# Optimization experiments

Hardware: AMD Instinct MI355X
Metric: run time of the kernel (lower is better)

The kernel has to match this reference:

```python
import jax, jax.numpy as jnp
import numpy as np

N_NODES = 50000
NEG_SLOPE = 0.2
EPS = 1e-16


def _gat_conv(x, src, dst, W, a_src, a_dst, bias, heads, out_c, concat):
    """PyG-style GATConv (self-loops assumed already added to src/dst)."""
    N = x.shape[0]
    h = (x @ W).reshape(N, heads, out_c)                 # [N,H,C]
    s_src = jnp.sum(h * a_src, axis=-1)                  # [N,H]
    s_dst = jnp.sum(h * a_dst, axis=-1)                  # [N,H]
    e = jax.nn.leaky_relu(s_src[src] + s_dst[dst], NEG_SLOPE)  # [E,H]
    # segment softmax over incoming edges of each dst node
    m = jax.ops.segment_max(e, dst, num_segments=N)      # [N,H]
    e = jnp.exp(e - m[dst])
    z = jax.ops.segment_sum(e, dst, num_segments=N)      # [N,H]
    alpha = e / (z[dst] + EPS)                           # [E,H]
    out = jax.ops.segment_sum(h[src] * alpha[:, :, None], dst, num_segments=N)  # [N,H,C]
    if concat:
        out = out.reshape(N, heads * out_c)
    else:
        out = out.mean(axis=1)
    return out + bias


def setup_inputs() -> dict:
    key = jax.random.key(0)
    ks = jax.random.split(key, 12)
    N, E, nfeat, nhid, nclass = N_NODES, 800000, 512, 256, 40
    heads, head_dim = 4, nhid // 4
    g = lambda k, shape, fan: (jax.random.normal(k, shape, jnp.float32) * (1.0 / np.sqrt(fan)))
    return {
        "x": jax.random.normal(ks[0], (N, nfeat), jnp.float32),
        "adj": jax.random.randint(ks[1], (2, E), 0, N, jnp.int64),
        "W1": g(ks[2], (nfeat, heads * head_dim), nfeat),
        "att_src1": g(ks[3], (heads, head_dim), head_dim),
        "att_dst1": g(ks[4], (heads, head_dim), head_dim),
        "b1": jnp.zeros((heads * head_dim,), jnp.float32),
        "W2": g(ks[5], (nhid, nclass), nhid),
        "att_src2": g(ks[6], (1, nclass), nclass),
        "att_dst2": g(ks[7], (1, nclass), nclass),
        "b2": jnp.zeros((nclass,), jnp.float32),
    }


def reference(x, adj, W1, att_src1, att_dst1, b1, W2, att_src2, att_dst2, b2):
    N = x.shape[0]
    loops = jnp.arange(N, dtype=adj.dtype)
    src = jnp.concatenate([adj[0], loops])   # PyG GATConv add_self_loops=True
    dst = jnp.concatenate([adj[1], loops])
    h = _gat_conv(x, src, dst, W1, att_src1, att_dst1, b1, heads=4, out_c=64, concat=True)
    h = jax.nn.relu(h)
    # dropout: eval mode => identity
    out = _gat_conv(h, src, dst, W2, att_src2, att_dst2, b2, heads=1, out_c=40, concat=False)
    return out
```

## Files before the change

kernel.cpp:

```cpp
#include <hip/hip_runtime.h>
#include <hip/hip_bf16.h>
#include <math.h>

#define NFEAT 512
#define NHID 256
#define HEADS 4
#define HDIM 64
#define NCLASS 40
#define NEG_SLOPE 0.2f
#define EPS_Z 1e-16f

typedef short bf16x8 __attribute__((ext_vector_type(8)));
typedef float f32x4 __attribute__((ext_vector_type(4)));

__device__ __forceinline__ float lrelu(float x) {
  return x > 0.f ? x : NEG_SLOPE * x;
}

__device__ __forceinline__ ushort f2bf(float f) {
  union { float f; uint u; } c; c.f = f;
  uint u = c.u;
  uint r = u + 0x7FFFu + ((u >> 16) & 1u);
  return (ushort)(r >> 16);
}
__device__ __forceinline__ float bf2f(ushort h) {
  union { uint u; float f; } c; c.u = ((uint)h) << 16;
  return c.f;
}

__device__ __forceinline__ uint cvtpk(float lo, float hi) {
  uint r;
  asm("v_cvt_pk_bf16_f32 %0, %1, %2" : "=v"(r) : "v"(lo), "v"(hi));
  return r;
}


__global__ void count_kernel(const int* __restrict__ dstv, int E, int* __restrict__ counts) {
  int i = blockIdx.x * blockDim.x + threadIdx.x;
  if (i < E) atomicAdd(&counts[dstv[i]], 1);
}

__global__ __launch_bounds__(1024) void scan_a(const int* __restrict__ counts,
    int* __restrict__ excl, int* __restrict__ bsum, int n) {
  __shared__ int tmp[1024];
  int t = threadIdx.x;
  int i = blockIdx.x * 1024 + t;
  int v = (i < n) ? counts[i] : 0;
  tmp[t] = v;
  __syncthreads();
  for (int off = 1; off < 1024; off <<= 1) {
    int u = (t >= off) ? tmp[t - off] : 0;
    __syncthreads();
    tmp[t] += u;
    __syncthreads();
  }
  if (i < n) excl[i] = tmp[t] - v;
  if (t == 1023) bsum[blockIdx.x] = tmp[t];
}

__global__ __launch_bounds__(1024) void scan_b(int* __restrict__ bsum, int nb) {
  __shared__ int tmp[1024];
  int t = threadIdx.x;
  tmp[t] = (t < nb) ? bsum[t] : 0;
  __syncthreads();
  for (int off = 1; off < 1024; off <<= 1) {
    int u = (t >= off) ? tmp[t - off] : 0;
    __syncthreads();
    tmp[t] += u;
    __syncthreads();
  }
  if (t < nb) bsum[t] = tmp[t];
}

__global__ void scan_c(const int* __restrict__ excl, const int* __restrict__ bsum_incl,
    int* __restrict__ row_off, int* __restrict__ cursor, int n, int E) {
  int i = blockIdx.x * blockDim.x + threadIdx.x;
  if (i < n) {
    int b = i >> 10;
    int off = (b > 0) ? bsum_incl[b - 1] : 0;
    int v = excl[i] + off;
    row_off[i] = v;
    cursor[i] = v;
  }
  if (i == 0) row_off[n] = E;
}

__global__ void scatter_kernel(const int* __restrict__ srcv, const int* __restrict__ dstv,
                               int E, int* __restrict__ cursor, int* __restrict__ edge_src) {
  int i = blockIdx.x * blockDim.x + threadIdx.x;
  if (i < E) {
    int pos = atomicAdd(&cursor[dstv[i]], 1);
    edge_src[pos] = srcv[i];
  }
}


__global__ __launch_bounds__(64) void wprep_kernel(const float* __restrict__ W,
    ushort* __restrict__ Bh) {
  int fb = blockIdx.x;
  int ct = fb >> 4, ks = fb & 15;
  int l = threadIdx.x;
  int g = l >> 4, rr = l & 15;
  uint hw[4];
  #pragma unroll
  for (int p = 0; p < 4; ++p) {
    ushort h2v[2];
    #pragma unroll
    for (int q = 0; q < 2; ++q) {
      int e = p * 2 + q;
      int k = ks * 32 + 4 * g + (e & 3) + 16 * (e >> 2);
      int col = ct * 16 + rr;
      h2v[q] = f2bf(W[k * NHID + col]);
    }
    hw[p] = (uint)h2v[0] | ((uint)h2v[1] << 16);
  }
  size_t o = ((size_t)fb * 64 + l) * 8;
  uint4 hv; hv.x = hw[0]; hv.y = hw[1]; hv.z = hw[2]; hv.w = hw[3];
  *(uint4*)&Bh[o] = hv;
}


__global__ __launch_bounds__(256, 4) void gemm1_mfma(const float* __restrict__ A,
    const ushort* __restrict__ Bh,
    const float* __restrict__ asrc, const float* __restrict__ adst,
    ushort* __restrict__ h1b, float* __restrict__ ssrc1, float* __restrict__ sdst1,
    int M) {
  __shared__ float A_s[2][64 * 64];
  const int tid = threadIdx.x;
  const int lane = tid & 63;
  const int wc = tid >> 6;
  const int g = lane >> 4, rr = lane & 15;
  const int row0 = blockIdx.x * 64;

  f32x4 acc[4][4] = {};

  auto stage = [&](int ki, int buf) {
    #pragma unroll
    for (int j = 0; j < 4; ++j) {
      int grp = wc * 4 + j;
      int s = grp * 64 + lane;
      int r = s >> 4;
      int us = s & 15;
      int ud = us ^ (r & 7);
      int gr = row0 + r;
      if (gr >= M) gr = M - 1;
      const float* src = &A[(size_t)gr * NFEAT + ki * 64 + ud * 4];
      float* dst = &A_s[buf][grp * 256];
      __builtin_amdgcn_global_load_lds(
          (const __attribute__((address_space(1))) float*)src,
          (__attribute__((address_space(3))) float*)dst, 16, 0, 0);
    }
  };

  stage(0, 0);
  __syncthreads();

  for (int ki = 0; ki < 8; ++ki) {
    const int cur = ki & 1;
    if (ki < 7) stage(ki + 1, cur ^ 1);

    #pragma unroll
    for (int kk = 0; kk < 2; ++kk) {
      const int ks = ki * 2 + kk;
      bf16x8 bhf[4];
      #pragma unroll
      for (int ni = 0; ni < 4; ++ni) {
        int ct = wc * 4 + ni;
        size_t bidx = ((size_t)(ct * 16 + ks) * 64 + lane) * 8;
        bhf[ni] = *(const bf16x8*)&Bh[bidx];
      }
      #pragma unroll
      for (int mi = 0; mi < 4; ++mi) {
        int row = mi * 16 + rr;
        int u0 = (8 * kk + g) ^ (row & 7);
        int u1 = (8 * kk + 4 + g) ^ (row & 7);
        f32x4 lo = *(const f32x4*)&A_s[cur][row * 64 + u0 * 4];
        f32x4 hi = *(const f32x4*)&A_s[cur][row * 64 + u1 * 4];
        uint w0 = cvtpk(lo[0], lo[1]);
        uint w1 = cvtpk(lo[2], lo[3]);
        uint w2 = cvtpk(hi[0], hi[1]);
        uint w3 = cvtpk(hi[2], hi[3]);
        union { uint u[4]; bf16x8 v; } af;
        af.u[0] = w0; af.u[1] = w1; af.u[2] = w2; af.u[3] = w3;
        #pragma unroll
        for (int ni = 0; ni < 4; ++ni) {
          acc[mi][ni] = __builtin_amdgcn_mfma_f32_16x16x32_bf16(af.v, bhf[ni], acc[mi][ni], 0, 0, 0);
        }
      }
    }
    __syncthreads();
  }

  float a_s[4], a_d[4];
  #pragma unroll
  for (int ni = 0; ni < 4; ++ni) {
    a_s[ni] = asrc[wc * 64 + ni * 16 + rr];
    a_d[ni] = adst[wc * 64 + ni * 16 + rr];
  }

  #pragma unroll
  for (int mi = 0; mi < 4; ++mi) {
    #pragma unroll
    for (int j = 0; j < 4; ++j) {
      int r = row0 + mi * 16 + g * 4 + j;
      bool ok = r < M;
      float ps = 0.f, pd = 0.f;
      #pragma unroll
      for (int ni = 0; ni < 4; ++ni) {
        float v = acc[mi][ni][j];
        ps += v * a_s[ni];
        pd += v * a_d[ni];
        if (ok) h1b[(size_t)r * NHID + wc * 64 + ni * 16 + rr] = f2bf(v);
      }
      #pragma unroll
      for (int m = 1; m < 16; m <<= 1) {
        ps += __shfl_xor(ps, m, 64);
        pd += __shfl_xor(pd, m, 64);
      }
      if (ok && rr == 0) {
        ssrc1[r * HEADS + wc] = ps;
        sdst1[r * HEADS + wc] = pd;
      }
    }
  }
}


__global__ __launch_bounds__(256) void gemm2_fused(const ushort* __restrict__ A,
    const float* __restrict__ B, const float* __restrict__ asrc,
    const float* __restrict__ adst, ushort* __restrict__ h2b,
    float* __restrict__ ssrc2, float* __restrict__ sdst2, int M) {
  __shared__ float As[16][64 + 1];
  __shared__ float Bs[16][68];
  const int tid = threadIdx.x;
  const int tx = tid & 15, ty = tid >> 4;
  const int row0 = blockIdx.x * 64;
  float acc[4][4] = {};

  const int la_r = tid >> 2;
  const int la_k = (tid & 3) * 4;
  const int lb_r = tid >> 4;
  const int lb_c = (tid & 15) * 4;

  for (int k0 = 0; k0 < NHID; k0 += 16) {
    float a0 = 0.f, a1 = 0.f, a2 = 0.f, a3 = 0.f;
    int ar = row0 + la_r;
    if (ar < M) {
      ushort4 uv = *(const ushort4*)&A[(size_t)ar * NHID + k0 + la_k];
      a0 = bf2f(uv.x); a1 = bf2f(uv.y); a2 = bf2f(uv.z); a3 = bf2f(uv.w);
    }
    As[la_k + 0][la_r] = a0;
    As[la_k + 1][la_r] = a1;
    As[la_k + 2][la_r] = a2;
    As[la_k + 3][la_r] = a3;

    float4 bv = make_float4(0.f, 0.f, 0.f, 0.f);
    const float* Brow = &B[(size_t)(k0 + lb_r) * NCLASS];
    if (lb_c + 3 < NCLASS) bv = *(const float4*)&Brow[lb_c];
    *(float4*)&Bs[lb_r][lb_c] = bv;
    __syncthreads();

    #pragma unroll
    for (int k = 0; k < 16; ++k) {
      float x0 = As[k][ty * 4 + 0];
      float x1 = As[k][ty * 4 + 1];
      float x2 = As[k][ty * 4 + 2];
      float x3 = As[k][ty * 4 + 3];
      float4 b = *(const float4*)&Bs[k][tx * 4];
      acc[0][0] += x0 * b.x; acc[0][1] += x0 * b.y; acc[0][2] += x0 * b.z; acc[0][3] += x0 * b.w;
      acc[1][0] += x1 * b.x; acc[1][1] += x1 * b.y; acc[1][2] += x1 * b.z; acc[1][3] += x1 * b.w;
      acc[2][0] += x2 * b.x; acc[2][1] += x2 * b.y; acc[2][2] += x2 * b.z; acc[2][3] += x2 * b.w;
      acc[3][0] += x3 * b.x; acc[3][1] += x3 * b.y; acc[3][2] += x3 * b.z; acc[3][3] += x3 * b.w;
    }
    __syncthreads();
  }

  const int cbase = tx * 4;
  const bool cok = cbase + 3 < NCLASS;
  float4 av_s = make_float4(0.f, 0.f, 0.f, 0.f);
  float4 av_d = make_float4(0.f, 0.f, 0.f, 0.f);
  if (cok) {
    av_s = *(const float4*)&asrc[cbase];
    av_d = *(const float4*)&adst[cbase];
  }

  #pragma unroll
  for (int i = 0; i < 4; ++i) {
    int r = row0 + ty * 4 + i;
    bool ok = r < M;
    float ps = acc[i][0] * av_s.x + acc[i][1] * av_s.y + acc[i][2] * av_s.z + acc[i][3] * av_s.w;
    float pd = acc[i][0] * av_d.x + acc[i][1] * av_d.y + acc[i][2] * av_d.z + acc[i][3] * av_d.w;
    #pragma unroll
    for (int m = 1; m < 16; m <<= 1) {
      ps += __shfl_xor(ps, m, 64);
      pd += __shfl_xor(pd, m, 64);
    }
    if (ok && cok) {
      ushort4 o;
      o.x = f2bf(acc[i][0]); o.y = f2bf(acc[i][1]);
      o.z = f2bf(acc[i][2]); o.w = f2bf(acc[i][3]);
      *(ushort4*)&h2b[(size_t)r * NCLASS + cbase] = o;
    }
    if (ok && tx == 0) { ssrc2[r] = ps; sdst2[r] = pd; }
  }
}


__global__ __launch_bounds__(64) void agg1_kernel(const ushort* __restrict__ h1b,
    const float* __restrict__ s_src, const float* __restrict__ s_dst,
    const int* __restrict__ row_off, const int* __restrict__ edge_src,
    const float* __restrict__ b1, ushort* __restrict__ hrelu_b) {
  int v = blockIdx.x;
  int l = threadIdx.x;
  int head = l >> 4;
  int c = l * 4;
  float sdv = s_dst[v * HEADS + head];

  float w = __expf(lrelu(s_src[v * HEADS + head] + sdv));
  ushort4 hv = *(const ushort4*)&h1b[(size_t)v * NHID + c];
  float4 acc = make_float4(w * bf2f(hv.x), w * bf2f(hv.y), w * bf2f(hv.z), w * bf2f(hv.w));
  float z = w;

  int i = row_off[v], end = row_off[v + 1];
  for (; i + 3 < end; i += 4) {
    int u0 = edge_src[i + 0];
    int u1 = edge_src[i + 1];
    int u2 = edge_src[i + 2];
    int u3 = edge_src[i + 3];
    float e0 = s_src[u0 * HEADS + head];
    float e1 = s_src[u1 * HEADS + head];
    float e2 = s_src[u2 * HEADS + head];
    float e3 = s_src[u3 * HEADS + head];
    ushort4 r0 = *(const ushort4*)&h1b[(size_t)u0 * NHID + c];
    ushort4 r1 = *(const ushort4*)&h1b[(size_t)u1 * NHID + c];
    ushort4 r2 = *(const ushort4*)&h1b[(size_t)u2 * NHID + c];
    ushort4 r3 = *(const ushort4*)&h1b[(size_t)u3 * NHID + c];
    float w0 = __expf(lrelu(e0 + sdv));
    float w1 = __expf(lrelu(e1 + sdv));
    float w2 = __expf(lrelu(e2 + sdv));
    float w3 = __expf(lrelu(e3 + sdv));
    acc.x += w0 * bf2f(r0.x) + w1 * bf2f(r1.x) + w2 * bf2f(r2.x) + w3 * bf2f(r3.x);
    acc.y += w0 * bf2f(r0.y) + w1 * bf2f(r1.y) + w2 * bf2f(r2.y) + w3 * bf2f(r3.y);
    acc.z += w0 * bf2f(r0.z) + w1 * bf2f(r1.z) + w2 * bf2f(r2.z) + w3 * bf2f(r3.z);
    acc.w += w0 * bf2f(r0.w) + w1 * bf2f(r1.w) + w2 * bf2f(r2.w) + w3 * bf2f(r3.w);
    z += (w0 + w1) + (w2 + w3);
  }
  for (; i < end; ++i) {
    int u = edge_src[i];
    float wu = __expf(lrelu(s_src[u * HEADS + head] + sdv));
    ushort4 hu = *(const ushort4*)&h1b[(size_t)u * NHID + c];
    acc.x += wu * bf2f(hu.x);
    acc.y += wu * bf2f(hu.y);
    acc.z += wu * bf2f(hu.z);
    acc.w += wu * bf2f(hu.w);
    z += wu;
  }
  float inv = 1.f / (z + EPS_Z);
  float4 bb = *(const float4*)&b1[c];
  ushort4 o;
  o.x = f2bf(fmaxf(acc.x * inv + bb.x, 0.f));
  o.y = f2bf(fmaxf(acc.y * inv + bb.y, 0.f));
  o.z = f2bf(fmaxf(acc.z * inv + bb.z, 0.f));
  o.w = f2bf(fmaxf(acc.w * inv + bb.w, 0.f));
  *(ushort4*)&hrelu_b[(size_t)v * NHID + c] = o;
}

__global__ __launch_bounds__(64) void agg2_kernel(const ushort* __restrict__ h2b,
    const float* __restrict__ s_src, const float* __restrict__ s_dst,
    const int* __restrict__ row_off, const int* __restrict__ edge_src,
    const float* __restrict__ b2, float* __restrict__ out) {
  int v = blockIdx.x;
  int l = threadIdx.x;
  bool act = l < NCLASS;
  float sdv = s_dst[v];

  float w = __expf(lrelu(s_src[v] + sdv));
  float acc = act ? w * bf2f(h2b[(size_t)v * NCLASS + l]) : 0.f;
  float z = w;

  int i = row_off[v], end = row_off[v + 1];
  for (; i + 3 < end; i += 4) {
    int u0 = edge_src[i + 0];
    int u1 = edge_src[i + 1];
    int u2 = edge_src[i + 2];
    int u3 = edge_src[i + 3];
    float e0 = s_src[u0];
    float e1 = s_src[u1];
    float e2 = s_src[u2];
    float e3 = s_src[u3];
    ushort p0 = 0, p1 = 0, p2 = 0, p3 = 0;
    if (act) {
      p0 = h2b[(size_t)u0 * NCLASS + l];
      p1 = h2b[(size_t)u1 * NCLASS + l];
      p2 = h2b[(size_t)u2 * NCLASS + l];
      p3 = h2b[(size_t)u3 * NCLASS + l];
    }
    float w0 = __expf(lrelu(e0 + sdv));
    float w1 = __expf(lrelu(e1 + sdv));
    float w2 = __expf(lrelu(e2 + sdv));
    float w3 = __expf(lrelu(e3 + sdv));
    if (act) acc += w0 * bf2f(p0) + w1 * bf2f(p1) + w2 * bf2f(p2) + w3 * bf2f(p3);
    z += (w0 + w1) + (w2 + w3);
  }
  for (; i < end; ++i) {
    int u = edge_src[i];
    float wu = __expf(lrelu(s_src[u] + sdv));
    if (act) acc += wu * bf2f(h2b[(size_t)u * NCLASS + l]);
    z += wu;
  }
  if (act) out[(size_t)v * NCLASS + l] = acc / (z + EPS_Z) + b2[l];
}


extern "C" void kernel_launch(void* const* d_in, const int* in_sizes, int n_in,
                              void* d_out, int out_size, void* d_ws, size_t ws_size,
                              hipStream_t stream) {
  const float* x   = (const float*)d_in[0];
  const int*   adj = (const int*)d_in[1];
  const float* W1  = (const float*)d_in[2];
  const float* as1 = (const float*)d_in[3];
  const float* ad1 = (const float*)d_in[4];
  const float* b1  = (const float*)d_in[5];
  const float* W2  = (const float*)d_in[6];
  const float* as2 = (const float*)d_in[7];
  const float* ad2 = (const float*)d_in[8];
  const float* b2  = (const float*)d_in[9];
  float* out = (float*)d_out;

  const int N = in_sizes[0] / NFEAT;
  const int E = in_sizes[1] / 2;

  char* ws = (char*)d_ws;
  size_t off = 0;
  auto alloc = [&](size_t bytes) -> void* {
    void* p = ws + off;
    off = (off + bytes + 255) & ~(size_t)255;
    return p;
  };
  ushort* h1b    = (ushort*)alloc((size_t)N * NHID * 2);
  ushort* hrelub = (ushort*)alloc((size_t)N * NHID * 2);
  ushort* h2b    = (ushort*)alloc((size_t)N * NCLASS * 2);
  float* ssrc1   = (float*)alloc((size_t)N * HEADS * 4);
  float* sdst1   = (float*)alloc((size_t)N * HEADS * 4);
  float* ssrc2   = (float*)alloc((size_t)N * 4);
  float* sdst2   = (float*)alloc((size_t)N * 4);
  int* counts    = (int*)alloc((size_t)N * 4);
  int* cursor    = (int*)alloc((size_t)N * 4);
  int* row_off   = (int*)alloc((size_t)(N + 1) * 4);
  int* edge_src  = (int*)alloc((size_t)E * 4);
  int* excl      = (int*)alloc((size_t)N * 4);
  int* bsum      = (int*)alloc((size_t)1024 * 4);
  ushort* whp    = (ushort*)alloc((size_t)NFEAT * NHID * 2);
  (void)ws_size;

  const int* srcv = adj;
  const int* dstv = adj + E;
  const int nb = (N + 1023) / 1024;

  wprep_kernel<<<256, 64, 0, stream>>>(W1, whp);

  hipMemsetAsync(counts, 0, (size_t)N * 4, stream);
  count_kernel<<<(E + 255) / 256, 256, 0, stream>>>(dstv, E, counts);
  scan_a<<<nb, 1024, 0, stream>>>(counts, excl, bsum, N);
  scan_b<<<1, 1024, 0, stream>>>(bsum, nb);
  scan_c<<<(N + 255) / 256, 256, 0, stream>>>(excl, bsum, row_off, cursor, N, E);
  scatter_kernel<<<(E + 255) / 256, 256, 0, stream>>>(srcv, dstv, E, cursor, edge_src);

  gemm1_mfma<<<(N + 63) / 64, 256, 0, stream>>>(x, whp, as1, ad1, h1b, ssrc1, sdst1, N);
  agg1_kernel<<<N, 64, 0, stream>>>(h1b, ssrc1, sdst1, row_off, edge_src, b1, hrelub);

  gemm2_fused<<<(N + 63) / 64, 256, 0, stream>>>(hrelub, W2, as2, ad2, h2b, ssrc2, sdst2, N);
  agg2_kernel<<<N, 64, 0, stream>>>(h2b, ssrc2, sdst2, row_off, edge_src, b2, out);
}
```

Baseline: 274.8 us.

## Cooperatively load edge indices and attention weights across lanes, broadcast via shuffles

In both aggregation kernels, each lane of the wavefront (or of its 16-lane head group) now loads one edge index and computes one exp attention weight for a chunk of edges. The index and weight are then broadcast with cross-lane shuffles while every lane gathers the feature rows. The softmax denominator becomes a per-lane partial that is reduced with xor-shuffles at the end. This removes the redundant per-lane loads of edge_src and s_src and the repeated exp computations. In exchange it adds shuffle traffic and an extra reduction.

```diff
diff --git a/kernel.cpp b/kernel.cpp
--- a/kernel.cpp
+++ b/kernel.cpp
@@ -313,49 +313,59 @@
   int v = blockIdx.x;
   int l = threadIdx.x;
   int head = l >> 4;
+  int elane = l & 15;
   int c = l * 4;
   float sdv = s_dst[v * HEADS + head];
 
-  float w = __expf(lrelu(s_src[v * HEADS + head] + sdv));
+  float wself = __expf(lrelu(s_src[v * HEADS + head] + sdv));
   ushort4 hv = *(const ushort4*)&h1b[(size_t)v * NHID + c];
-  float4 acc = make_float4(w * bf2f(hv.x), w * bf2f(hv.y), w * bf2f(hv.z), w * bf2f(hv.w));
-  float z = w;
+  float4 acc = make_float4(wself * bf2f(hv.x), wself * bf2f(hv.y),
+                           wself * bf2f(hv.z), wself * bf2f(hv.w));
+  float zp = (elane == 0) ? wself : 0.f;
 
   int i = row_off[v], end = row_off[v + 1];
-  for (; i + 3 < end; i += 4) {
-    int u0 = edge_src[i + 0];
-    int u1 = edge_src[i + 1];
-    int u2 = edge_src[i + 2];
-    int u3 = edge_src[i + 3];
-    float e0 = s_src[u0 * HEADS + head];
-    float e1 = s_src[u1 * HEADS + head];
-    float e2 = s_src[u2 * HEADS + head];
-    float e3 = s_src[u3 * HEADS + head];
-    ushort4 r0 = *(const ushort4*)&h1b[(size_t)u0 * NHID + c];
-    ushort4 r1 = *(const ushort4*)&h1b[(size_t)u1 * NHID + c];
-    ushort4 r2 = *(const ushort4*)&h1b[(size_t)u2 * NHID + c];
-    ushort4 r3 = *(const ushort4*)&h1b[(size_t)u3 * NHID + c];
-    float w0 = __expf(lrelu(e0 + sdv));
-    float w1 = __expf(lrelu(e1 + sdv));
-    float w2 = __expf(lrelu(e2 + sdv));
-    float w3 = __expf(lrelu(e3 + sdv));
-    acc.x += w0 * bf2f(r0.x) + w1 * bf2f(r1.x) + w2 * bf2f(r2.x) + w3 * bf2f(r3.x);
-    acc.y += w0 * bf2f(r0.y) + w1 * bf2f(r1.y) + w2 * bf2f(r2.y) + w3 * bf2f(r3.y);
-    acc.z += w0 * bf2f(r0.z) + w1 * bf2f(r1.z) + w2 * bf2f(r2.z) + w3 * bf2f(r3.z);
-    acc.w += w0 * bf2f(r0.w) + w1 * bf2f(r1.w) + w2 * bf2f(r2.w) + w3 * bf2f(r3.w);
-    z += (w0 + w1) + (w2 + w3);
-  }
-  for (; i < end; ++i) {
-    int u = edge_src[i];
-    float wu = __expf(lrelu(s_src[u * HEADS + head] + sdv));
-    ushort4 hu = *(const ushort4*)&h1b[(size_t)u * NHID + c];
-    acc.x += wu * bf2f(hu.x);
-    acc.y += wu * bf2f(hu.y);
-    acc.z += wu * bf2f(hu.z);
-    acc.w += wu * bf2f(hu.w);
-    z += wu;
-  }
-  float inv = 1.f / (z + EPS_Z);
+  for (; i < end; i += 16) {
+    int cnt = end - i;
+    if (cnt > 16) cnt = 16;
+    bool val = elane < cnt;
+    int u = edge_src[val ? (i + elane) : i];
+    float wl = 0.f;
+    if (val) wl = __expf(lrelu(s_src[u * HEADS + head] + sdv));
+    zp += wl;
+
+    int e = 0;
+    for (; e + 3 < cnt; e += 4) {
+      int u0 = __shfl(u, e + 0);
+      int u1 = __shfl(u, e + 1);
+      int u2 = __shfl(u, e + 2);
+      int u3 = __shfl(u, e + 3);
+      float w0 = __shfl(wl, (l & 48) | (e + 0));
+      float w1 = __shfl(wl, (l & 48) | (e + 1));
+      float w2 = __shfl(wl, (l & 48) | (e + 2));
+      float w3 = __shfl(wl, (l & 48) | (e + 3));
+      ushort4 r0 = *(const ushort4*)&h1b[(size_t)u0 * NHID + c];
+      ushort4 r1 = *(const ushort4*)&h1b[(size_t)u1 * NHID + c];
+      ushort4 r2 = *(const ushort4*)&h1b[(size_t)u2 * NHID + c];
+      ushort4 r3 = *(const ushort4*)&h1b[(size_t)u3 * NHID + c];
+      acc.x += w0 * bf2f(r0.x) + w1 * bf2f(r1.x) + w2 * bf2f(r2.x) + w3 * bf2f(r3.x);
+      acc.y += w0 * bf2f(r0.y) + w1 * bf2f(r1.y) + w2 * bf2f(r2.y) + w3 * bf2f(r3.y);
+      acc.z += w0 * bf2f(r0.z) + w1 * bf2f(r1.z) + w2 * bf2f(r2.z) + w3 * bf2f(r3.z);
+      acc.w += w0 * bf2f(r0.w) + w1 * bf2f(r1.w) + w2 * bf2f(r2.w) + w3 * bf2f(r3.w);
+    }
+    for (; e < cnt; ++e) {
+      int ue = __shfl(u, e);
+      float we = __shfl(wl, (l & 48) | e);
+      ushort4 ru = *(const ushort4*)&h1b[(size_t)ue * NHID + c];
+      acc.x += we * bf2f(ru.x);
+      acc.y += we * bf2f(ru.y);
+      acc.z += we * bf2f(ru.z);
+      acc.w += we * bf2f(ru.w);
+    }
+  }
+  #pragma unroll
+  for (int m = 1; m < 16; m <<= 1) zp += __shfl_xor(zp, m, 64);
+
+  float inv = 1.f / (zp + EPS_Z);
   float4 bb = *(const float4*)&b1[c];
   ushort4 o;
   o.x = f2bf(fmaxf(acc.x * inv + bb.x, 0.f));
@@ -374,41 +384,49 @@
   bool act = l < NCLASS;
   float sdv = s_dst[v];
 
-  float w = __expf(lrelu(s_src[v] + sdv));
-  float acc = act ? w * bf2f(h2b[(size_t)v * NCLASS + l]) : 0.f;
-  float z = w;
+  float wself = __expf(lrelu(s_src[v] + sdv));
+  float acc = act ? wself * bf2f(h2b[(size_t)v * NCLASS + l]) : 0.f;
+  float zp = (l == 0) ? wself : 0.f;
 
   int i = row_off[v], end = row_off[v + 1];
-  for (; i + 3 < end; i += 4) {
-    int u0 = edge_src[i + 0];
-    int u1 = edge_src[i + 1];
-    int u2 = edge_src[i + 2];
-    int u3 = edge_src[i + 3];
-    float e0 = s_src[u0];
-    float e1 = s_src[u1];
-    float e2 = s_src[u2];
-    float e3 = s_src[u3];
-    ushort p0 = 0, p1 = 0, p2 = 0, p3 = 0;
-    if (act) {
-      p0 = h2b[(size_t)u0 * NCLASS + l];
-      p1 = h2b[(size_t)u1 * NCLASS + l];
-      p2 = h2b[(size_t)u2 * NCLASS + l];
-      p3 = h2b[(size_t)u3 * NCLASS + l];
-    }
-    float w0 = __expf(lrelu(e0 + sdv));
-    float w1 = __expf(lrelu(e1 + sdv));
-    float w2 = __expf(lrelu(e2 + sdv));
-    float w3 = __expf(lrelu(e3 + sdv));
-    if (act) acc += w0 * bf2f(p0) + w1 * bf2f(p1) + w2 * bf2f(p2) + w3 * bf2f(p3);
-    z += (w0 + w1) + (w2 + w3);
-  }
-  for (; i < end; ++i) {
-    int u = edge_src[i];
-    float wu = __expf(lrelu(s_src[u] + sdv));
-    if (act) acc += wu * bf2f(h2b[(size_t)u * NCLASS + l]);
-    z += wu;
-  }
-  if (act) out[(size_t)v * NCLASS + l] = acc / (z + EPS_Z) + b2[l];
+  for (; i < end; i += 64) {
+    int cnt = end - i;
+    if (cnt > 64) cnt = 64;
+    bool val = l < cnt;
+    int u = edge_src[val ? (i + l) : i];
+    float wl = 0.f;
+    if (val) wl = __expf(lrelu(s_src[u] + sdv));
+    zp += wl;
+
+    int e = 0;
+    for (; e + 3 < cnt; e += 4) {
+      int u0 = __shfl(u, e + 0);
+      int u1 = __shfl(u, e + 1);
+      int u2 = __shfl(u, e + 2);
+      int u3 = __shfl(u, e + 3);
+      float w0 = __shfl(wl, e + 0);
+      float w1 = __shfl(wl, e + 1);
+      float w2 = __shfl(wl, e + 2);
+      float w3 = __shfl(wl, e + 3);
+      ushort p0 = 0, p1 = 0, p2 = 0, p3 = 0;
+      if (act) {
+        p0 = h2b[(size_t)u0 * NCLASS + l];
+        p1 = h2b[(size_t)u1 * NCLASS + l];
+        p2 = h2b[(size_t)u2 * NCLASS + l];
+        p3 = h2b[(size_t)u3 * NCLASS + l];
+      }
+      if (act) acc += w0 * bf2f(p0) + w1 * bf2f(p1) + w2 * bf2f(p2) + w3 * bf2f(p3);
+    }
+    for (; e < cnt; ++e) {
+      int ue = __shfl(u, e);
+      float we = __shfl(wl, e);
+      if (act) acc += we * bf2f(h2b[(size_t)ue * NCLASS + l]);
+    }
+  }
+  #pragma unroll
+  for (int m = 1; m < 64; m <<= 1) zp += __shfl_xor(zp, m, 64);
+
+  if (act) out[(size_t)v * NCLASS + l] = acc / (zp + EPS_Z) + b2[l];
 }
 
 
```

After: 268.9 us (median of 2 runs). 1.02x faster.
